# Kernel tuning notes

Hardware: AMD Instinct MI355X
Metric: run time of the kernel (lower is better)

Reference implementation:

```python
import jax, jax.numpy as jnp
from jax import lax
import numpy as np

B, C_IN, H, W = 256, 2, 15, 15
DIM_MID, DIM_OUT = 128, 64
N_RES = 4  # DirectionalConvResBlocks

# tap positions inside a 3x3 kernel for each of the 4 line directions
# (matches DirectionalConvLayer.weight_func_map: horiz, vert, diag, anti-diag)
_POS = (((1, 0), (1, 1), (1, 2)),
        ((0, 1), (1, 1), (2, 1)),
        ((0, 0), (1, 1), (2, 2)),
        ((2, 0), (1, 1), (0, 2)))


def _dir_kernel(w3, d):
    # w3: [3, O, I] -> [O, I, 3, 3] with taps placed along direction d
    O, I = w3.shape[1], w3.shape[2]
    kern = jnp.zeros((O, I, 3, 3), w3.dtype)
    for k, (r, c) in enumerate(_POS[d]):
        kern = kern.at[:, :, r, c].set(w3[k])
    return kern


def _dconv(x, w3, b, d):
    kern = _dir_kernel(w3, d)
    y = lax.conv_general_dilated(x, kern, window_strides=(1, 1),
                                 padding=((1, 1), (1, 1)),
                                 dimension_numbers=('NCHW', 'OIHW', 'NCHW'))
    return y + b[None, :, None, None]


def _pw(x, w, b):
    # 1x1 conv: w [O, I]
    return jnp.einsum('bihw,oi->bohw', x, w) + b[None, :, None, None]


def setup_inputs() -> dict:
    key = jax.random.key(0)
    ks = jax.random.split(key, 16)
    s_in = 1.0 / np.sqrt(3 * C_IN)
    s_mid = 1.0 / np.sqrt(3 * DIM_MID)
    s_pw = 1.0 / np.sqrt(DIM_MID)
    return {
        'x': jax.random.normal(ks[0], (B, C_IN, H, W), jnp.float32),
        'dconv0_w': jax.random.normal(ks[1], (3, DIM_MID, C_IN), jnp.float32) * s_in,
        'dconv0_b': jnp.zeros((DIM_MID,), jnp.float32),
        'rb_dconv_w': jax.random.normal(ks[2], (N_RES, 3, DIM_MID, DIM_MID), jnp.float32) * s_mid,
        'rb_dconv_b': jnp.zeros((N_RES, DIM_MID), jnp.float32),
        'rb_c1_w': jax.random.normal(ks[3], (N_RES, DIM_MID, DIM_MID), jnp.float32) * s_pw,
        'rb_c1_b': jnp.zeros((N_RES, DIM_MID), jnp.float32),
        'c0_w1': jax.random.normal(ks[4], (DIM_MID, DIM_MID), jnp.float32) * s_pw,
        'c0_b1': jnp.zeros((DIM_MID,), jnp.float32),
        'c0_w2': jax.random.normal(ks[5], (DIM_MID, DIM_MID), jnp.float32) * s_pw,
        'c0_b2': jnp.zeros((DIM_MID,), jnp.float32),
        'final_w': jax.random.normal(ks[6], (DIM_OUT, DIM_MID), jnp.float32) * s_pw,
        'final_b': jnp.zeros((DIM_OUT,), jnp.float32),
    }


def reference(x, dconv0_w, dconv0_b, rb_dconv_w, rb_dconv_b, rb_c1_w, rb_c1_b,
              c0_w1, c0_b1, c0_w2, c0_b2, final_w, final_b):
    silu = jax.nn.silu
    outs = []
    for d in range(4):  # 4 board directions, shared weights
        h = silu(_dconv(x, dconv0_w, dconv0_b, d))
        for i in range(N_RES):  # DirectionalConvResBlock
            r = h
            h = silu(_dconv(h, rb_dconv_w[i], rb_dconv_b[i], d))
            h = silu(_pw(h, rb_c1_w[i], rb_c1_b[i]))
            h = h + r
        # Conv0dResBlock
        r = h
        h = silu(_pw(h, c0_w1, c0_b1))
        h = silu(_pw(h, c0_w2, c0_b2))
        h = h + r
        outs.append(_pw(h, final_w, final_b))
    return jnp.stack(outs, axis=1)  # [B, 4, DIM_OUT, H, W]
```

## Files before the change

### kernel.cpp

```cpp
#include <hip/hip_runtime.h>
#include <cstdint>
#include <cstddef>


#define HWX 15
#define NPOS 225
#define CH 128
#define NTH 512
#define AROWB 80
#define ABYTES (CH*AROWB)
#define HOFF2 ABYTES
#define GRID_SLOTS 273
#define LDS_BYTES (ABYTES + GRID_SLOTS*256)
#define SAFE_PP 136

typedef _Float16 f16;
typedef __attribute__((ext_vector_type(8))) _Float16 f16x8;
typedef __attribute__((ext_vector_type(4))) _Float16 f16x4;
typedef __attribute__((ext_vector_type(4))) float f32x4;

__device__ __forceinline__ int hb_addr(int pp, int k){
  return HOFF2 + pp*256 + ((k*2) ^ ((pp&15)<<4));
}
__device__ __forceinline__ int a_addr(int o, int k){
  return o*AROWB + k*2;
}
__device__ __forceinline__ float silu_f(float v){ return v / (1.f + __expf(-v)); }

__device__ __forceinline__ void stage_a(char* sm, const float* __restrict__ src,
                                        int srcStride, int rows, int tid){
  const int o = tid >> 2, kq = tid & 3;
  if (o < rows){
    const float* s = src + (size_t)o*srcStride + kq*8;
    float4 fa = *(const float4*)(s);
    float4 fb = *(const float4*)(s + 4);
    f16x8 hv = { (f16)fa.x,(f16)fa.y,(f16)fa.z,(f16)fa.w,
                 (f16)fb.x,(f16)fb.y,(f16)fb.z,(f16)fb.w };
    *(f16x8*)(sm + a_addr(o, kq*8)) = hv;
  }
}

template<int MT>
__device__ __forceinline__ void gemm32(const char* sm, int pb0, int pb1, int ks,
                                       int krow, int col, f32x4* acc0, f32x4* acc1){
  const int k8 = krow*8;
  f16x8 b0 = *(const f16x8*)(sm + hb_addr(pb0, ks + k8));
  f16x8 b1 = *(const f16x8*)(sm + hb_addr(pb1, ks + k8));
#pragma unroll
  for (int mt=0; mt<MT; mt++){
    f16x8 a = *(const f16x8*)(sm + a_addr(mt*16+col, k8));
    acc0[mt] = __builtin_amdgcn_mfma_f32_16x16x32_f16(a, b0, acc0[mt], 0, 0, 0);
    acc1[mt] = __builtin_amdgcn_mfma_f32_16x16x32_f16(a, b1, acc1[mt], 0, 0, 0);
  }
}

template<int MT>
__device__ __forceinline__ void pw_pass(char* sm, const float* __restrict__ w,
                                        int rows, int pb0, int pb1,
                                        int krow, int col, int tid,
                                        f32x4* acc0, f32x4* acc1){
#pragma unroll 1
  for (int ks=0; ks<CH; ks+=32){
    __syncthreads();
    stage_a(sm, w + ks, CH, rows, tid);
    __syncthreads();
    gemm32<MT>(sm, pb0, pb1, ks, krow, col, acc0, acc1);
  }
}

template<int MT>
__device__ __forceinline__ void zacc(f32x4* a){
#pragma unroll
  for (int m=0;m<MT;m++) a[m] = (f32x4){0.f,0.f,0.f,0.f};
}

__device__ __forceinline__ void snap8(const char* sm, f16x4* r, int pp, int krow){
#pragma unroll
  for (int mt=0;mt<8;mt++)
    r[mt] = *(const f16x4*)(sm + hb_addr(pp, mt*16 + krow*4));
}

template<int MT, bool SILU, bool RES>
__device__ __forceinline__ void wb(char* sm, const f32x4* acc,
                                   const float* __restrict__ bias,
                                   const f16x4* rsd, int pp, bool valid, int krow){
#pragma unroll
  for (int mt=0;mt<MT;mt++){
    const int ch0 = mt*16 + krow*4;
    float4 bb = *(const float4*)(bias + ch0);
    f32x4 v = acc[mt];
    v[0]+=bb.x; v[1]+=bb.y; v[2]+=bb.z; v[3]+=bb.w;
    if (SILU){
#pragma unroll
      for (int j=0;j<4;j++) v[j] = silu_f(v[j]);
    }
    if (RES){
      f16x4 r = rsd[mt];
#pragma unroll
      for (int j=0;j<4;j++) v[j] += (float)r[j];
    }
    if (valid){
      f16x4 o = { (f16)v[0],(f16)v[1],(f16)v[2],(f16)v[3] };
      *(f16x4*)(sm + hb_addr(pp, ch0)) = o;
    }
  }
}

struct P {
  const float *x, *w0, *b0, *wdc, *bdc, *wc1, *bc1, *w01, *b01, *w02, *b02, *wf, *bf;
};

__global__ __launch_bounds__(NTH, 4)
void mix9_mfma2(const P p, float* __restrict__ out)
{
  __shared__ char sm[LDS_BYTES];
  const int tid  = threadIdx.x;
  const int lane = tid & 63;
  const int wave = tid >> 6;
  const int col  = lane & 15;
  const int krow = lane >> 4;
  const int d = blockIdx.x & 3;
  const int b = blockIdx.x >> 2;

  for (int i = tid; i < LDS_BYTES/16; i += NTH)
    ((f32x4*)sm)[i] = (f32x4){0.f,0.f,0.f,0.f};
  __syncthreads();

  for (int i = tid; i < 2*NPOS; i += NTH){
    const int ic = i / NPOS, n = i % NPOS;
    const int pp = (n/HWX + 1)*16 + (n%HWX + 1);
    *(f16*)(sm + hb_addr(pp, ic)) = (f16)p.x[(size_t)b*2*NPOS + i];
  }

  const int r0 = wave*2, r1 = wave*2 + 1;
  const bool v0 = (col >= 1);
  const bool v1 = (col >= 1) && (r1 < HWX);
  const int pb0 = v0 ? (r0+1)*16 + col : SAFE_PP;
  const int pb1 = v1 ? (r1+1)*16 + col : SAFE_PP;

  int dneg;
  switch (d){
    case 0:  dneg = -1;  break;
    case 1:  dneg = -16; break;
    case 2:  dneg = -17; break;
    default: dneg =  15; break;
  }
  const int tap[3] = { dneg, 0, -dneg };

  f32x4 acc0[8], acc1[8];
  f16x4 rsd0[8], rsd1[8];

  zacc<8>(acc0); zacc<8>(acc1);
#pragma unroll 1
  for (int k=0;k<3;k++){
    __syncthreads();
    if (tid < 256)
      *(f16*)(sm + a_addr(tid>>1, tid&1)) = (f16)p.w0[k*256 + tid];
    __syncthreads();
    gemm32<8>(sm, pb0+tap[k], pb1+tap[k], 0, krow, col, acc0, acc1);
  }
  __syncthreads();
  wb<8,true,false>(sm, acc0, p.b0, nullptr, pb0, v0, krow);
  wb<8,true,false>(sm, acc1, p.b0, nullptr, pb1, v1, krow);

#pragma unroll 1
  for (int res=0; res<4; res++){
    const float* wd = p.wdc + (size_t)res*3*CH*CH;
    zacc<8>(acc0); zacc<8>(acc1);
#pragma unroll 1
    for (int k=0;k<3;k++){
#pragma unroll 1
      for (int ks=0; ks<CH; ks+=32){
        __syncthreads();
        stage_a(sm, wd + (size_t)k*CH*CH + ks, CH, CH, tid);
        __syncthreads();
        gemm32<8>(sm, pb0+tap[k], pb1+tap[k], ks, krow, col, acc0, acc1);
      }
    }
    __syncthreads();
    snap8(sm, rsd0, pb0, krow);
    snap8(sm, rsd1, pb1, krow);
    wb<8,true,false>(sm, acc0, p.bdc + res*CH, nullptr, pb0, v0, krow);
    wb<8,true,false>(sm, acc1, p.bdc + res*CH, nullptr, pb1, v1, krow);

    zacc<8>(acc0); zacc<8>(acc1);
    pw_pass<8>(sm, p.wc1 + (size_t)res*CH*CH, CH, pb0, pb1, krow, col, tid, acc0, acc1);
    __syncthreads();
    wb<8,true,true>(sm, acc0, p.bc1 + res*CH, rsd0, pb0, v0, krow);
    wb<8,true,true>(sm, acc1, p.bc1 + res*CH, rsd1, pb1, v1, krow);
  }

  zacc<8>(acc0); zacc<8>(acc1);
  pw_pass<8>(sm, p.w01, CH, pb0, pb1, krow, col, tid, acc0, acc1);
  __syncthreads();
  snap8(sm, rsd0, pb0, krow);
  snap8(sm, rsd1, pb1, krow);
  wb<8,true,false>(sm, acc0, p.b01, nullptr, pb0, v0, krow);
  wb<8,true,false>(sm, acc1, p.b01, nullptr, pb1, v1, krow);

  zacc<8>(acc0); zacc<8>(acc1);
  pw_pass<8>(sm, p.w02, CH, pb0, pb1, krow, col, tid, acc0, acc1);
  __syncthreads();
  wb<8,true,true>(sm, acc0, p.b02, rsd0, pb0, v0, krow);
  wb<8,true,true>(sm, acc1, p.b02, rsd1, pb1, v1, krow);

  zacc<4>(acc0); zacc<4>(acc1);
  pw_pass<4>(sm, p.wf, 64, pb0, pb1, krow, col, tid, acc0, acc1);

  float* ob = out + ((size_t)(b*4 + d)*64)*NPOS;
  const int nb0 = r0*HWX + (col-1);
  const int nb1 = r1*HWX + (col-1);
#pragma unroll
  for (int mt=0;mt<4;mt++){
    const int ch0 = mt*16 + krow*4;
    float4 bb = *(const float4*)(p.bf + ch0);
    const float bj[4] = {bb.x, bb.y, bb.z, bb.w};
#pragma unroll
    for (int j=0;j<4;j++){
      if (v0) ob[(size_t)(ch0+j)*NPOS + nb0] = acc0[mt][j] + bj[j];
      if (v1) ob[(size_t)(ch0+j)*NPOS + nb1] = acc1[mt][j] + bj[j];
    }
  }
}

extern "C" void kernel_launch(void* const* d_in, const int* in_sizes, int n_in,
                              void* d_out, int out_size, void* d_ws, size_t ws_size,
                              hipStream_t stream)
{
  (void)in_sizes; (void)n_in; (void)d_ws; (void)ws_size; (void)out_size;
  P p;
  p.x   = (const float*)d_in[0];
  p.w0  = (const float*)d_in[1];
  p.b0  = (const float*)d_in[2];
  p.wdc = (const float*)d_in[3];
  p.bdc = (const float*)d_in[4];
  p.wc1 = (const float*)d_in[5];
  p.bc1 = (const float*)d_in[6];
  p.w01 = (const float*)d_in[7];
  p.b01 = (const float*)d_in[8];
  p.w02 = (const float*)d_in[9];
  p.b02 = (const float*)d_in[10];
  p.wf  = (const float*)d_in[11];
  p.bf  = (const float*)d_in[12];

  mix9_mfma2<<<dim3(256*4), dim3(NTH), 0, stream>>>(p, (float*)d_out);
}
```

Baseline: 595.1 us.

## Pre-convert weights to fp16 blocks and give each wave four rows

A prepass kernel converts all fp32 weights into packed fp16 blocks laid out per 32-wide k-slice in the workspace, so the main kernel loads half-precision tiles directly. The main kernel halves the block to 256 threads, and each wave now computes four spatial rows, which reuses every A-tile fragment across four MFMAs. It also adds register double-buffering of the weight stage and an XOR-swizzled A layout in LDS. The trade-offs are more accumulator registers (launch bounds drop to 2 blocks), fewer waves to hide latency, and an extra launch per call.

```diff
diff --git a/kernel.cpp b/kernel.cpp
--- a/kernel.cpp
+++ b/kernel.cpp
@@ -6,13 +6,20 @@
 #define HWX 15
 #define NPOS 225
 #define CH 128
-#define NTH 512
-#define AROWB 80
-#define ABYTES (CH*AROWB)
-#define HOFF2 ABYTES
+#define NTH 256
+#define ABYTES 8192
+#define HOFF ABYTES
 #define GRID_SLOTS 273
 #define LDS_BYTES (ABYTES + GRID_SLOTS*256)
 #define SAFE_PP 136
+
+#define WSE_WDC 0
+#define WSE_WC1 196608
+#define WSE_W01 262144
+#define WSE_W02 278528
+#define WSE_WF  294912
+#define WSE_TOTAL 303104
+#define WS_NEED (WSE_TOTAL*2)
 
 typedef _Float16 f16;
 typedef __attribute__((ext_vector_type(8))) _Float16 f16x8;
@@ -20,88 +27,129 @@
 typedef __attribute__((ext_vector_type(4))) float f32x4;
 
 __device__ __forceinline__ int hb_addr(int pp, int k){
-  return HOFF2 + pp*256 + ((k*2) ^ ((pp&15)<<4));
+  return HOFF + pp*256 + ((k*2) ^ ((pp&15)<<4));
 }
 __device__ __forceinline__ int a_addr(int o, int k){
-  return o*AROWB + k*2;
+  return o*64 + ((((k>>3))<<4) ^ ((o&3)<<4)) + ((k&7)*2);
 }
 __device__ __forceinline__ float silu_f(float v){ return v / (1.f + __expf(-v)); }
 
-__device__ __forceinline__ void stage_a(char* sm, const float* __restrict__ src,
-                                        int srcStride, int rows, int tid){
-  const int o = tid >> 2, kq = tid & 3;
-  if (o < rows){
-    const float* s = src + (size_t)o*srcStride + kq*8;
-    float4 fa = *(const float4*)(s);
-    float4 fb = *(const float4*)(s + 4);
-    f16x8 hv = { (f16)fa.x,(f16)fa.y,(f16)fa.z,(f16)fa.w,
-                 (f16)fb.x,(f16)fb.y,(f16)fb.z,(f16)fb.w };
-    *(f16x8*)(sm + a_addr(o, kq*8)) = hv;
+struct StReg { f16x8 a, b; bool on; };
+
+template<bool WS>
+__device__ __forceinline__ StReg stage_load(const f16* __restrict__ wsblk,
+                                            const float* __restrict__ f32p,
+                                            int stride, int rows, int tid){
+  StReg r;
+  const int o = tid>>1, kh = tid&1;
+  r.on = (o < rows);
+  if (r.on){
+    if (WS){
+      r.a = *(const f16x8*)(wsblk + o*32 + kh*16);
+      r.b = *(const f16x8*)(wsblk + o*32 + kh*16 + 8);
+    } else {
+      const float* s = f32p + (size_t)o*stride + kh*16;
+      float4 x0 = *(const float4*)(s);
+      float4 x1 = *(const float4*)(s+4);
+      float4 x2 = *(const float4*)(s+8);
+      float4 x3 = *(const float4*)(s+12);
+      r.a = (f16x8){(f16)x0.x,(f16)x0.y,(f16)x0.z,(f16)x0.w,
+                    (f16)x1.x,(f16)x1.y,(f16)x1.z,(f16)x1.w};
+      r.b = (f16x8){(f16)x2.x,(f16)x2.y,(f16)x2.z,(f16)x2.w,
+                    (f16)x3.x,(f16)x3.y,(f16)x3.z,(f16)x3.w};
+    }
+  }
+  return r;
+}
+
+__device__ __forceinline__ void stage_write(char* sm, StReg r, int tid){
+  const int o = tid>>1, kh = tid&1;
+  if (r.on){
+    *(f16x8*)(sm + a_addr(o, kh*16))   = r.a;
+    *(f16x8*)(sm + a_addr(o, kh*16+8)) = r.b;
   }
 }
 
 template<int MT>
-__device__ __forceinline__ void gemm32(const char* sm, int pb0, int pb1, int ks,
-                                       int krow, int col, f32x4* acc0, f32x4* acc1){
-  const int k8 = krow*8;
-  f16x8 b0 = *(const f16x8*)(sm + hb_addr(pb0, ks + k8));
-  f16x8 b1 = *(const f16x8*)(sm + hb_addr(pb1, ks + k8));
+__device__ __forceinline__ void gemm32(const char* sm, const int* pbs, int ks,
+                                       int krow, int col, f32x4 acc[4][8]){
+  const int kb = ks + krow*8;
+  const int ka = krow*8;
+  f16x8 b0 = *(const f16x8*)(sm + hb_addr(pbs[0], kb));
+  f16x8 b1 = *(const f16x8*)(sm + hb_addr(pbs[1], kb));
+  f16x8 b2 = *(const f16x8*)(sm + hb_addr(pbs[2], kb));
+  f16x8 b3 = *(const f16x8*)(sm + hb_addr(pbs[3], kb));
 #pragma unroll
   for (int mt=0; mt<MT; mt++){
-    f16x8 a = *(const f16x8*)(sm + a_addr(mt*16+col, k8));
-    acc0[mt] = __builtin_amdgcn_mfma_f32_16x16x32_f16(a, b0, acc0[mt], 0, 0, 0);
-    acc1[mt] = __builtin_amdgcn_mfma_f32_16x16x32_f16(a, b1, acc1[mt], 0, 0, 0);
-  }
-}
-
-template<int MT>
-__device__ __forceinline__ void pw_pass(char* sm, const float* __restrict__ w,
-                                        int rows, int pb0, int pb1,
-                                        int krow, int col, int tid,
-                                        f32x4* acc0, f32x4* acc1){
+    f16x8 a = *(const f16x8*)(sm + a_addr(mt*16+col, ka));
+    acc[0][mt] = __builtin_amdgcn_mfma_f32_16x16x32_f16(a, b0, acc[0][mt], 0,0,0);
+    acc[1][mt] = __builtin_amdgcn_mfma_f32_16x16x32_f16(a, b1, acc[1][mt], 0,0,0);
+    acc[2][mt] = __builtin_amdgcn_mfma_f32_16x16x32_f16(a, b2, acc[2][mt], 0,0,0);
+    acc[3][mt] = __builtin_amdgcn_mfma_f32_16x16x32_f16(a, b3, acc[3][mt], 0,0,0);
+  }
+}
+
+template<int MT, bool WS>
+__device__ __forceinline__ void pw_pass(char* sm, const f16* __restrict__ wsblk,
+                                        const float* __restrict__ f32p,
+                                        int stride, int rows, const int* pbs,
+                                        int krow, int col, int tid, f32x4 acc[4][8]){
+  StReg cur = stage_load<WS>(wsblk, f32p, stride, rows, tid);
 #pragma unroll 1
   for (int ks=0; ks<CH; ks+=32){
     __syncthreads();
-    stage_a(sm, w + ks, CH, rows, tid);
-    __syncthreads();
-    gemm32<MT>(sm, pb0, pb1, ks, krow, col, acc0, acc1);
-  }
-}
-
-template<int MT>
-__device__ __forceinline__ void zacc(f32x4* a){
-#pragma unroll
-  for (int m=0;m<MT;m++) a[m] = (f32x4){0.f,0.f,0.f,0.f};
-}
-
-__device__ __forceinline__ void snap8(const char* sm, f16x4* r, int pp, int krow){
-#pragma unroll
-  for (int mt=0;mt<8;mt++)
-    r[mt] = *(const f16x4*)(sm + hb_addr(pp, mt*16 + krow*4));
+    stage_write(sm, cur, tid);
+    if (ks+32 < CH)
+      cur = stage_load<WS>(wsblk + (ks/32+1)*rows*32, f32p + ks + 32, stride, rows, tid);
+    __syncthreads();
+    gemm32<MT>(sm, pbs, ks, krow, col, acc);
+  }
+}
+
+__device__ __forceinline__ void zacc_all(f32x4 acc[4][8]){
+#pragma unroll
+  for (int t=0;t<4;t++)
+#pragma unroll
+    for (int m=0;m<8;m++) acc[t][m] = (f32x4){0.f,0.f,0.f,0.f};
+}
+
+__device__ __forceinline__ void snap4x8(const char* sm, f16x4 r[4][8],
+                                        const int* pbs, int krow){
+#pragma unroll
+  for (int t=0;t<4;t++)
+#pragma unroll
+    for (int mt=0;mt<8;mt++)
+      r[t][mt] = *(const f16x4*)(sm + hb_addr(pbs[t], mt*16 + krow*4));
 }
 
 template<int MT, bool SILU, bool RES>
-__device__ __forceinline__ void wb(char* sm, const f32x4* acc,
-                                   const float* __restrict__ bias,
-                                   const f16x4* rsd, int pp, bool valid, int krow){
+__device__ __forceinline__ void wb4(char* sm, f32x4 acc[4][8],
+                                    const float* __restrict__ bias,
+                                    f16x4 rsd[4][8], const int* pbs,
+                                    const bool* val, int krow){
 #pragma unroll
   for (int mt=0;mt<MT;mt++){
     const int ch0 = mt*16 + krow*4;
     float4 bb = *(const float4*)(bias + ch0);
-    f32x4 v = acc[mt];
-    v[0]+=bb.x; v[1]+=bb.y; v[2]+=bb.z; v[3]+=bb.w;
-    if (SILU){
-#pragma unroll
-      for (int j=0;j<4;j++) v[j] = silu_f(v[j]);
-    }
-    if (RES){
-      f16x4 r = rsd[mt];
-#pragma unroll
-      for (int j=0;j<4;j++) v[j] += (float)r[j];
-    }
-    if (valid){
-      f16x4 o = { (f16)v[0],(f16)v[1],(f16)v[2],(f16)v[3] };
-      *(f16x4*)(sm + hb_addr(pp, ch0)) = o;
+    const float bj[4] = {bb.x, bb.y, bb.z, bb.w};
+#pragma unroll
+    for (int t=0;t<4;t++){
+      f32x4 v = acc[t][mt];
+#pragma unroll
+      for (int j=0;j<4;j++) v[j] += bj[j];
+      if (SILU){
+#pragma unroll
+        for (int j=0;j<4;j++) v[j] = silu_f(v[j]);
+      }
+      if (RES){
+        f16x4 r = rsd[t][mt];
+#pragma unroll
+        for (int j=0;j<4;j++) v[j] += (float)r[j];
+      }
+      if (val[t]){
+        f16x4 o = { (f16)v[0],(f16)v[1],(f16)v[2],(f16)v[3] };
+        *(f16x4*)(sm + hb_addr(pbs[t], ch0)) = o;
+      }
     }
   }
 }
@@ -110,8 +158,9 @@
   const float *x, *w0, *b0, *wdc, *bdc, *wc1, *bc1, *w01, *b01, *w02, *b02, *wf, *bf;
 };
 
-__global__ __launch_bounds__(NTH, 4)
-void mix9_mfma2(const P p, float* __restrict__ out)
+template<bool WS>
+__global__ __launch_bounds__(NTH, 2)
+void mix9_v3(const P p, const f16* __restrict__ wsf, float* __restrict__ out)
 {
   __shared__ char sm[LDS_BYTES];
   const int tid  = threadIdx.x;
@@ -127,17 +176,18 @@
   __syncthreads();
 
   for (int i = tid; i < 2*NPOS; i += NTH){
-    const int ic = i / NPOS, n = i % NPOS;
+    const int ic = i/NPOS, n = i%NPOS;
     const int pp = (n/HWX + 1)*16 + (n%HWX + 1);
     *(f16*)(sm + hb_addr(pp, ic)) = (f16)p.x[(size_t)b*2*NPOS + i];
   }
 
-  const int r0 = wave*2, r1 = wave*2 + 1;
-  const bool v0 = (col >= 1);
-  const bool v1 = (col >= 1) && (r1 < HWX);
-  const int pb0 = v0 ? (r0+1)*16 + col : SAFE_PP;
-  const int pb1 = v1 ? (r1+1)*16 + col : SAFE_PP;
-
+  int pbs[4]; bool val[4];
+#pragma unroll
+  for (int t=0;t<4;t++){
+    const int r = wave*4 + t;
+    val[t] = (col >= 1) && (r < HWX);
+    pbs[t] = val[t] ? (r+1)*16 + col : SAFE_PP;
+  }
   int dneg;
   switch (d){
     case 0:  dneg = -1;  break;
@@ -145,89 +195,120 @@
     case 2:  dneg = -17; break;
     default: dneg =  15; break;
   }
-  const int tap[3] = { dneg, 0, -dneg };
-
-  f32x4 acc0[8], acc1[8];
-  f16x4 rsd0[8], rsd1[8];
-
-  zacc<8>(acc0); zacc<8>(acc1);
+
+  f32x4 acc[4][8];
+  f16x4 rsd[4][8];
+
+  zacc_all(acc);
 #pragma unroll 1
   for (int k=0;k<3;k++){
-    __syncthreads();
-    if (tid < 256)
-      *(f16*)(sm + a_addr(tid>>1, tid&1)) = (f16)p.w0[k*256 + tid];
-    __syncthreads();
-    gemm32<8>(sm, pb0+tap[k], pb1+tap[k], 0, krow, col, acc0, acc1);
+    const int sh = (k==0) ? dneg : (k==1) ? 0 : -dneg;
+    int pbt[4];
+#pragma unroll
+    for (int t=0;t<4;t++) pbt[t] = pbs[t] + sh;
+    __syncthreads();
+    *(f16*)(sm + a_addr(tid>>1, tid&1)) = (f16)p.w0[k*256 + tid];
+    __syncthreads();
+    gemm32<8>(sm, pbt, 0, krow, col, acc);
   }
   __syncthreads();
-  wb<8,true,false>(sm, acc0, p.b0, nullptr, pb0, v0, krow);
-  wb<8,true,false>(sm, acc1, p.b0, nullptr, pb1, v1, krow);
+  wb4<8,true,false>(sm, acc, p.b0, nullptr, pbs, val, krow);
 
 #pragma unroll 1
   for (int res=0; res<4; res++){
-    const float* wd = p.wdc + (size_t)res*3*CH*CH;
-    zacc<8>(acc0); zacc<8>(acc1);
+    zacc_all(acc);
 #pragma unroll 1
     for (int k=0;k<3;k++){
-#pragma unroll 1
-      for (int ks=0; ks<CH; ks+=32){
-        __syncthreads();
-        stage_a(sm, wd + (size_t)k*CH*CH + ks, CH, CH, tid);
-        __syncthreads();
-        gemm32<8>(sm, pb0+tap[k], pb1+tap[k], ks, krow, col, acc0, acc1);
-      }
+      const int sh = (k==0) ? dneg : (k==1) ? 0 : -dneg;
+      int pbt[4];
+#pragma unroll
+      for (int t=0;t<4;t++) pbt[t] = pbs[t] + sh;
+      const f16* blk = wsf + WSE_WDC + (size_t)(res*3 + k)*4*4096;
+      const float* fp = p.wdc + (size_t)(res*3 + k)*CH*CH;
+      pw_pass<8,WS>(sm, blk, fp, CH, CH, pbt, krow, col, tid, acc);
     }
     __syncthreads();
-    snap8(sm, rsd0, pb0, krow);
-    snap8(sm, rsd1, pb1, krow);
-    wb<8,true,false>(sm, acc0, p.bdc + res*CH, nullptr, pb0, v0, krow);
-    wb<8,true,false>(sm, acc1, p.bdc + res*CH, nullptr, pb1, v1, krow);
-
-    zacc<8>(acc0); zacc<8>(acc1);
-    pw_pass<8>(sm, p.wc1 + (size_t)res*CH*CH, CH, pb0, pb1, krow, col, tid, acc0, acc1);
-    __syncthreads();
-    wb<8,true,true>(sm, acc0, p.bc1 + res*CH, rsd0, pb0, v0, krow);
-    wb<8,true,true>(sm, acc1, p.bc1 + res*CH, rsd1, pb1, v1, krow);
-  }
-
-  zacc<8>(acc0); zacc<8>(acc1);
-  pw_pass<8>(sm, p.w01, CH, pb0, pb1, krow, col, tid, acc0, acc1);
+    snap4x8(sm, rsd, pbs, krow);
+    wb4<8,true,false>(sm, acc, p.bdc + res*CH, nullptr, pbs, val, krow);
+
+    zacc_all(acc);
+    pw_pass<8,WS>(sm, wsf + WSE_WC1 + (size_t)res*4*4096,
+                  p.wc1 + (size_t)res*CH*CH, CH, CH, pbs, krow, col, tid, acc);
+    __syncthreads();
+    wb4<8,true,true>(sm, acc, p.bc1 + res*CH, rsd, pbs, val, krow);
+  }
+
+  zacc_all(acc);
+  pw_pass<8,WS>(sm, wsf + WSE_W01, p.w01, CH, CH, pbs, krow, col, tid, acc);
   __syncthreads();
-  snap8(sm, rsd0, pb0, krow);
-  snap8(sm, rsd1, pb1, krow);
-  wb<8,true,false>(sm, acc0, p.b01, nullptr, pb0, v0, krow);
-  wb<8,true,false>(sm, acc1, p.b01, nullptr, pb1, v1, krow);
-
-  zacc<8>(acc0); zacc<8>(acc1);
-  pw_pass<8>(sm, p.w02, CH, pb0, pb1, krow, col, tid, acc0, acc1);
+  snap4x8(sm, rsd, pbs, krow);
+  wb4<8,true,false>(sm, acc, p.b01, nullptr, pbs, val, krow);
+
+  zacc_all(acc);
+  pw_pass<8,WS>(sm, wsf + WSE_W02, p.w02, CH, CH, pbs, krow, col, tid, acc);
   __syncthreads();
-  wb<8,true,true>(sm, acc0, p.b02, rsd0, pb0, v0, krow);
-  wb<8,true,true>(sm, acc1, p.b02, rsd1, pb1, v1, krow);
-
-  zacc<4>(acc0); zacc<4>(acc1);
-  pw_pass<4>(sm, p.wf, 64, pb0, pb1, krow, col, tid, acc0, acc1);
+  wb4<8,true,true>(sm, acc, p.b02, rsd, pbs, val, krow);
+
+  zacc_all(acc);
+  pw_pass<4,WS>(sm, wsf + WSE_WF, p.wf, CH, 64, pbs, krow, col, tid, acc);
 
   float* ob = out + ((size_t)(b*4 + d)*64)*NPOS;
-  const int nb0 = r0*HWX + (col-1);
-  const int nb1 = r1*HWX + (col-1);
-#pragma unroll
-  for (int mt=0;mt<4;mt++){
-    const int ch0 = mt*16 + krow*4;
-    float4 bb = *(const float4*)(p.bf + ch0);
-    const float bj[4] = {bb.x, bb.y, bb.z, bb.w};
-#pragma unroll
-    for (int j=0;j<4;j++){
-      if (v0) ob[(size_t)(ch0+j)*NPOS + nb0] = acc0[mt][j] + bj[j];
-      if (v1) ob[(size_t)(ch0+j)*NPOS + nb1] = acc1[mt][j] + bj[j];
+#pragma unroll
+  for (int t=0;t<4;t++){
+    const int r = wave*4 + t;
+    const int n = r*HWX + (col-1);
+#pragma unroll
+    for (int mt=0;mt<4;mt++){
+      const int ch0 = mt*16 + krow*4;
+      float4 bb = *(const float4*)(p.bf + ch0);
+      const float bj[4] = {bb.x, bb.y, bb.z, bb.w};
+#pragma unroll
+      for (int j=0;j<4;j++)
+        if (val[t]) ob[(size_t)(ch0+j)*NPOS + n] = acc[t][mt][j] + bj[j];
     }
   }
+}
+
+__global__ void cvt_ws(const P p, f16* __restrict__ ws)
+{
+  const int idx = blockIdx.x*NTH + threadIdx.x;
+  if (idx >= WSE_TOTAL) return;
+  float v;
+  if (idx < WSE_WC1){
+    int blk = idx >> 12, rem = idx & 4095;
+    int o = rem >> 5, k = rem & 31;
+    int ks = blk & 3, tapres = blk >> 2;
+    v = p.wdc[((size_t)tapres*CH + o)*CH + ks*32 + k];
+  } else if (idx < WSE_W01){
+    int j = idx - WSE_WC1;
+    int blk = j >> 12, rem = j & 4095;
+    int o = rem >> 5, k = rem & 31;
+    int ks = blk & 3, res = blk >> 2;
+    v = p.wc1[((size_t)res*CH + o)*CH + ks*32 + k];
+  } else if (idx < WSE_W02){
+    int j = idx - WSE_W01;
+    int ks = j >> 12, rem = j & 4095;
+    int o = rem >> 5, k = rem & 31;
+    v = p.w01[(size_t)o*CH + ks*32 + k];
+  } else if (idx < WSE_WF){
+    int j = idx - WSE_W02;
+    int ks = j >> 12, rem = j & 4095;
+    int o = rem >> 5, k = rem & 31;
+    v = p.w02[(size_t)o*CH + ks*32 + k];
+  } else {
+    int j = idx - WSE_WF;
+    int ks = j >> 11, rem = j & 2047;
+    int o = rem >> 5, k = rem & 31;
+    v = p.wf[(size_t)o*CH + ks*32 + k];
+  }
+  ws[idx] = (f16)v;
 }
 
 extern "C" void kernel_launch(void* const* d_in, const int* in_sizes, int n_in,
                               void* d_out, int out_size, void* d_ws, size_t ws_size,
                               hipStream_t stream)
 {
-  (void)in_sizes; (void)n_in; (void)d_ws; (void)ws_size; (void)out_size;
+  (void)in_sizes; (void)n_in; (void)out_size;
   P p;
   p.x   = (const float*)d_in[0];
   p.w0  = (const float*)d_in[1];
@@ -243,5 +324,14 @@
   p.wf  = (const float*)d_in[11];
   p.bf  = (const float*)d_in[12];
 
-  mix9_mfma2<<<dim3(256*4), dim3(NTH), 0, stream>>>(p, (float*)d_out);
-}
+  float* out = (float*)d_out;
+  const bool ws_ok = (d_ws != nullptr) && (ws_size >= (size_t)WS_NEED);
+
+  if (ws_ok){
+    f16* ws = (f16*)d_ws;
+    cvt_ws<<<dim3((WSE_TOTAL + NTH - 1)/NTH), dim3(NTH), 0, stream>>>(p, ws);
+    mix9_v3<true><<<dim3(256*4), dim3(NTH), 0, stream>>>(p, ws, out);
+  } else {
+    mix9_v3<false><<<dim3(256*4), dim3(NTH), 0, stream>>>(p, nullptr, out);
+  }
+}
```

Measured after the change: 518.5 us. -12.9%, faster.
